# Optimization experiments

Measured on AMD Instinct MI355X. Metric: run time of the kernel, lower is better.

The kernel has to match this reference:

```python
import jax, jax.numpy as jnp
import numpy as np

# dims
B, L, H, NH, D = 512, 200, 128, 4, 32      # batch, seq_len, hidden, heads (gnn & fcb), head dim H/NH
FT, TP, IP = 32, 64, 200                    # first_taxonomy_num, taxonomy/item nodes per graph
NHOP, NB = 2, 2                             # n_hop gnn layers, gip_block_nums
SH, FH = 512, 256                           # scb_hidden_units, fcb_hidden_units
ITEMS, TAX = 100001, 2000                   # item vocab (+pad row 0), taxonomy vocab
NT, NI = B * TP, B * IP                     # total taxonomy / item nodes in batched forest
DEG_I, DEG_T = 4, 2                         # in-degree per taxonomy node for i2t / t2t edges


def _ln(x, g, b, eps=1e-8):
    m = jnp.mean(x, -1, keepdims=True)
    v = jnp.mean((x - m) ** 2, -1, keepdims=True)
    return (x - m) / jnp.sqrt(v + eps) * g + b


def _gat(src_h, dst_h, es, ed, W, al, ar, bias):
    """DGL GATConv (eval mode): shared fc, leaky_relu(0.2) scores, segment softmax,
    identity residual (in == heads*out), bias, ReLU activation."""
    fs = (src_h @ W).reshape(-1, NH, D)                 # [Ns,NH,D]
    fd = (dst_h @ W).reshape(-1, NH, D)                 # [Nd,NH,D]
    el = jnp.sum(fs * al, -1)                           # [Ns,NH]
    er = jnp.sum(fd * ar, -1)                           # [Nd,NH]
    e = jax.nn.leaky_relu(el[es] + er[ed], 0.2)         # [E,NH]
    emax = jax.ops.segment_max(e, ed, num_segments=NT)
    a = jnp.exp(e - emax[ed])
    s = jax.ops.segment_sum(a, ed, num_segments=NT)
    alpha = a / s[ed]                                   # [E,NH]
    rst = jax.ops.segment_sum(alpha[..., None] * fs[es], ed, num_segments=NT)
    rst = rst + dst_h.reshape(-1, NH, D) + bias.reshape(NH, D)
    return jax.nn.relu(rst).reshape(-1, NH * D)


def _forward(item_embed, tax_embed, scb_ln_g, scb_ln_b, scb_w1, scb_w2, fcb_ln_g, fcb_ln_b,
             fcb_w1, fcb_w2, fcb_w3, wv, gi_w, gi_al, gi_ar, gi_b, gt_w, gt_al, gt_ar, gt_b,
             liw_g, liw_b, int_g, int_b, uni_w,
             seq, root, i2t_src, i2t_dst, t2t_src, t2t_dst, item_ids, tax_ids):
    # --- global intention: mixer-style blocks over the item sequence ---
    V = item_embed[seq]                                           # [B,L,H]
    for i in range(NB):
        nv = _ln(V, scb_ln_g[i], scb_ln_b[i])
        t = jax.nn.gelu(jnp.einsum('blh,ls->bhs', nv, scb_w1[i]), approximate=False)
        vs = nv + jnp.einsum('bhs,sl->blh', t, scb_w2[i])         # seq-mixing block
        nvs = _ln(vs, fcb_ln_g[i], fcb_ln_b[i])
        xh = nvs.reshape(B, L, NH, D)                             # fcb heads share w1/w2
        y = jax.nn.gelu(jnp.einsum('blkc,cf->blkf', xh, fcb_w1[i]), approximate=False)
        y = jnp.einsum('blkf,fc->blkc', y, fcb_w2[i]).reshape(B, L, H)
        V = nvs + y @ fcb_w3[i]
    alpha = jax.nn.softmax(V @ wv, axis=1)                        # [B,L]
    g = jnp.sum(alpha[..., None] * V, axis=1)                     # [B,H]
    # --- local intention: multi-hop hetero GAT on batched item-taxonomy forest ---
    item_h = item_embed[item_ids]                                 # [NI,H]
    tax_h = tax_embed[tax_ids]                                    # [NT,H]
    acc = jnp.zeros_like(tax_h)
    for hop in range(NHOP):
        t_i = _gat(item_h, tax_h, i2t_src, i2t_dst, gi_w[hop], gi_al[hop], gi_ar[hop], gi_b[hop])
        t_t = _gat(tax_h, tax_h, t2t_src, t2t_dst, gt_w[hop], gt_al[hop], gt_ar[hop], gt_b[hop])
        tax_h = t_i + t_t                                         # HeteroGraphConv 'sum'
        acc = acc + tax_h                                         # k_list accumulation
    total = acc / NHOP                                            # average over hops
    offs = jnp.arange(B) * TP                                     # batched-graph offsets (graph_taxonomy)
    valid = root != -1
    local = jnp.where(valid[..., None], total[jnp.clip(root, 0) + offs[:, None]], 0.0)  # [B,FT,H]
    # --- fuse global + local ---
    mul = jnp.einsum('bfh,bh->bf', local, g)                      # [B,FT]
    w = jax.nn.softmax(jnp.where(mul != 0, _ln(mul, liw_g, liw_b), -jnp.inf), axis=-1)
    intention = _ln(g + jnp.sum(w[..., None] * local, axis=1), int_g, int_b)
    return (intention @ uni_w) @ item_embed.T                     # [B, ITEMS]


def setup_inputs():
    key = jax.random.key(0)
    ks = jax.random.split(key, 32)
    nrm = lambda i, sh: jax.random.normal(ks[i], sh, jnp.float32) * 0.05
    inp = {}
    inp['seq'] = jax.random.randint(ks[0], (B, L), 0, ITEMS)
    inp['root'] = jax.random.randint(ks[1], (B, FT), 0, TP)       # all valid roots
    i2t_dst = jnp.repeat(jnp.arange(NT), DEG_I)
    inp['i2t_dst'] = i2t_dst
    inp['i2t_src'] = (i2t_dst // TP) * IP + jax.random.randint(ks[2], (NT * DEG_I,), 0, IP)
    t2t_dst = jnp.repeat(jnp.arange(NT), DEG_T)
    inp['t2t_dst'] = t2t_dst
    inp['t2t_src'] = (t2t_dst // TP) * TP + jax.random.randint(ks[3], (NT * DEG_T,), 0, TP)
    inp['item_ids'] = jax.random.randint(ks[4], (NI,), 1, ITEMS)
    inp['tax_ids'] = jax.random.randint(ks[5], (NT,), 1, TAX)
    inp['item_embed'] = nrm(6, (ITEMS, H)).at[0].set(0.0)         # padding_idx=0
    inp['tax_embed'] = nrm(7, (TAX, H)).at[0].set(0.0)
    inp['scb_ln_g'] = jnp.ones((NB, H)); inp['scb_ln_b'] = jnp.zeros((NB, H))
    inp['scb_w1'] = nrm(8, (NB, L, SH)); inp['scb_w2'] = nrm(9, (NB, SH, L))
    inp['fcb_ln_g'] = jnp.ones((NB, H)); inp['fcb_ln_b'] = jnp.zeros((NB, H))
    inp['fcb_w1'] = nrm(10, (NB, D, FH)); inp['fcb_w2'] = nrm(11, (NB, FH, D))
    inp['fcb_w3'] = nrm(12, (NB, H, H))
    inp['wv'] = nrm(13, (H,))
    inp['gi_w'] = nrm(14, (NHOP, H, H)); inp['gi_al'] = nrm(15, (NHOP, NH, D))
    inp['gi_ar'] = nrm(16, (NHOP, NH, D)); inp['gi_b'] = nrm(17, (NHOP, H))
    inp['gt_w'] = nrm(18, (NHOP, H, H)); inp['gt_al'] = nrm(19, (NHOP, NH, D))
    inp['gt_ar'] = nrm(20, (NHOP, NH, D)); inp['gt_b'] = nrm(21, (NHOP, H))
    inp['liw_g'] = jnp.ones((FT,)); inp['liw_b'] = jnp.zeros((FT,))
    inp['int_g'] = jnp.ones((H,)); inp['int_b'] = jnp.zeros((H,))
    inp['uni_w'] = nrm(22, (H, H))
    return inp


def reference(item_embed, tax_embed, scb_ln_g, scb_ln_b, scb_w1, scb_w2, fcb_ln_g, fcb_ln_b,
              fcb_w1, fcb_w2, fcb_w3, wv, gi_w, gi_al, gi_ar, gi_b, gt_w, gt_al, gt_ar, gt_b,
              liw_g, liw_b, int_g, int_b, uni_w,
              seq, root, i2t_src, i2t_dst, t2t_src, t2t_dst, item_ids, tax_ids):
    return _forward(item_embed, tax_embed, scb_ln_g, scb_ln_b, scb_w1, scb_w2, fcb_ln_g, fcb_ln_b,
                    fcb_w1, fcb_w2, fcb_w3, wv, gi_w, gi_al, gi_ar, gi_b, gt_w, gt_al, gt_ar, gt_b,
                    liw_g, liw_b, int_g, int_b, uni_w,
                    seq, root, i2t_src, i2t_dst, t2t_src, t2t_dst, item_ids, tax_ids)
```

## Files before the change

kernel.cpp:

```cpp
#include <hip/hip_runtime.h>
#include <hip/hip_bf16.h>

constexpr int TB = 512, TL = 200, TH = 128, TNH = 4, TD = 32;
constexpr int TFT = 32, TTP = 64, TIP = 200;
constexpr int TSH = 512, TFH = 256;
constexpr int TITEMS = 100001;
constexpr int TNT = TB * TTP;
constexpr int TNI = TB * TIP;
constexpr int TLP = 224;
constexpr int TIPAD = 100096;

typedef __attribute__((ext_vector_type(8))) short short8v;
typedef __attribute__((ext_vector_type(4))) float f32x4;

__device__ inline float gelu_fast(float x) {
    float u = x + 0.044715f * x * x * x;
    float e = exp2f(-2.302208f * u);
    return x / (1.0f + e);
}
__device__ inline unsigned short to_bf16u(float x) {
    __hip_bfloat16 h = __float2bfloat16(x);
    return *reinterpret_cast<unsigned short*>(&h);
}
__device__ inline float bfu_to_f(unsigned short u) {
    unsigned int x = ((unsigned int)u) << 16;
    return __uint_as_float(x);
}

__device__ inline float block_reduce_sum(float v, float* red) {
    for (int o = 32; o > 0; o >>= 1) v += __shfl_down(v, o, 64);
    int nw = blockDim.x >> 6;
    if ((threadIdx.x & 63) == 0) red[threadIdx.x >> 6] = v;
    __syncthreads();
    float r = 0.f;
    for (int w = 0; w < nw; ++w) r += red[w];
    __syncthreads();
    return r;
}

__global__ __launch_bounds__(256) void k_gather(const float* __restrict__ tab,
                                                const int* __restrict__ idx,
                                                float* __restrict__ out, int nrows) {
    int e = blockIdx.x * blockDim.x + threadIdx.x;
    if (e >= nrows * 32) return;
    int r = e >> 5, c = e & 31;
    ((float4*)out)[e] = ((const float4*)tab)[(size_t)idx[r] * 32 + c];
}

__global__ __launch_bounds__(256) void k_gather_bf(const float* __restrict__ tab,
                                                   const int* __restrict__ idx,
                                                   unsigned short* __restrict__ out, int nrows) {
    int e = blockIdx.x * blockDim.x + threadIdx.x;
    if (e >= nrows * 16) return;
    int r = e >> 4, c = e & 15;
    const float4 a = ((const float4*)tab)[(size_t)idx[r] * 32 + c * 2];
    const float4 b = ((const float4*)tab)[(size_t)idx[r] * 32 + c * 2 + 1];
    uint4 u;
    u.x = (unsigned int)to_bf16u(a.x) | ((unsigned int)to_bf16u(a.y) << 16);
    u.y = (unsigned int)to_bf16u(a.z) | ((unsigned int)to_bf16u(a.w) << 16);
    u.z = (unsigned int)to_bf16u(b.x) | ((unsigned int)to_bf16u(b.y) << 16);
    u.w = (unsigned int)to_bf16u(b.z) | ((unsigned int)to_bf16u(b.w) << 16);
    *(uint4*)(out + (size_t)e * 8) = u;
}

__global__ __launch_bounds__(256) void k_wcvt(const float* __restrict__ fw1, const float* __restrict__ fw2,
                                              const float* __restrict__ fw3, const float* __restrict__ giw,
                                              const float* __restrict__ gtw, unsigned short* __restrict__ WB) {
    int idx = blockIdx.x * 256 + threadIdx.x;
    float v;
    if (idx < 16384) {
        int nb = idx >> 13, r = idx & 8191, n = r >> 5, k = r & 31;
        v = fw1[(size_t)nb * 8192 + k * 256 + n];
    } else if (idx < 32768) {
        int t = idx - 16384;
        int nb = t >> 13, r = t & 8191, n = r >> 8, k = r & 255;
        v = fw2[(size_t)nb * 8192 + k * 32 + n];
    } else if (idx < 65536) {
        int t = idx - 32768;
        int nb = t >> 14, r = t & 16383, n = r >> 7, k = r & 127;
        v = fw3[(size_t)nb * 16384 + k * 128 + n];
    } else if (idx < 98304) {
        int t = idx - 65536;
        int hop = t >> 14, r = t & 16383, n = r >> 7, k = r & 127;
        v = giw[(size_t)hop * 16384 + k * 128 + n];
    } else {
        int t = idx - 98304;
        int hop = t >> 14, r = t & 16383, n = r >> 7, k = r & 127;
        v = gtw[(size_t)hop * 16384 + k * 128 + n];
    }
    WB[idx] = to_bf16u(v);
}

__global__ __launch_bounds__(128) void k_lnt(const float* __restrict__ V,
                                             const float* __restrict__ g, const float* __restrict__ b,
                                             float* __restrict__ NV, unsigned short* __restrict__ NVT) {
    __shared__ float tl[64][129];
    __shared__ float mrow[64], irow[64];
    int bb = blockIdx.y, l0 = blockIdx.x * 64, tid = threadIdx.x;
    for (int i = tid; i < 2048; i += 128) {
        int r = i >> 5, c = i & 31;
        int l = l0 + r;
        float4 v = {0.f, 0.f, 0.f, 0.f};
        if (l < TL) v = *(const float4*)(V + ((size_t)bb * TL + l) * TH + c * 4);
        tl[r][c * 4 + 0] = v.x; tl[r][c * 4 + 1] = v.y;
        tl[r][c * 4 + 2] = v.z; tl[r][c * 4 + 3] = v.w;
    }
    __syncthreads();
    {
        int row = tid >> 1, half = tid & 1;
        float s = 0.f, sq = 0.f;
        for (int k = 0; k < 64; ++k) {
            float v = tl[row][half * 64 + k];
            s += v; sq += v * v;
        }
        s += __shfl_xor(s, 1);
        sq += __shfl_xor(sq, 1);
        if (half == 0) {
            float mean = s * (1.f / 128.f);
            mrow[row] = mean;
            irow[row] = rsqrtf(sq * (1.f / 128.f) - mean * mean + 1e-8f);
        }
    }
    __syncthreads();
    for (int i = tid; i < 2048; i += 128) {
        int r = i >> 5, c = i & 31;
        int l = l0 + r;
        float4 o = {0.f, 0.f, 0.f, 0.f};
        if (l < TL) {
            float4 v = *(float4*)&tl[r][c * 4];
            float m = mrow[r], inv = irow[r];
            const float4 gg = ((const float4*)g)[c];
            const float4 bv = ((const float4*)b)[c];
            o.x = (v.x - m) * inv * gg.x + bv.x;
            o.y = (v.y - m) * inv * gg.y + bv.y;
            o.z = (v.z - m) * inv * gg.z + bv.z;
            o.w = (v.w - m) * inv * gg.w + bv.w;
            *(float4*)(NV + ((size_t)bb * TL + l) * TH + c * 4) = o;
        }
        *(float4*)&tl[r][c * 4] = o;
    }
    __syncthreads();
    int h = tid;
    int ng = (l0 + 64 > TLP) ? (TLP - l0) / 8 : 8;
    for (int lg = 0; lg < ng; ++lg) {
        uint4 u;
        unsigned int p[4];
#pragma unroll
        for (int q = 0; q < 4; ++q) {
            unsigned short ua = to_bf16u(tl[lg * 8 + q * 2 + 0][h]);
            unsigned short ub = to_bf16u(tl[lg * 8 + q * 2 + 1][h]);
            p[q] = (unsigned int)ua | ((unsigned int)ub << 16);
        }
        u.x = p[0]; u.y = p[1]; u.z = p[2]; u.w = p[3];
        *(uint4*)(NVT + ((size_t)bb * TH + h) * TLP + l0 + lg * 8) = u;
    }
}

__global__ __launch_bounds__(256) void k_wscb(const float* __restrict__ w1, const float* __restrict__ w2,
                                              unsigned short* __restrict__ W1T,
                                              unsigned short* __restrict__ W2T) {
    int bx = blockIdx.x;
    if (bx < TSH) {
        int s = bx, l = threadIdx.x;
        if (l < TLP) W1T[(size_t)s * TLP + l] = to_bf16u(l < TL ? w1[(size_t)l * TSH + s] : 0.f);
    } else {
        int l = bx - TSH;
        for (int it = 0; it < 2; ++it) {
            int s = it * 256 + threadIdx.x;
            W2T[(size_t)l * TSH + s] = to_bf16u(l < TL ? w2[(size_t)s * TL + l] : 0.f);
        }
    }
}

__global__ __launch_bounds__(256) void k_mm1(const unsigned short* __restrict__ NVT,
                                             const unsigned short* __restrict__ W1T,
                                             unsigned short* __restrict__ T, int bh) {
    __shared__ unsigned short As[128][40];
    __shared__ unsigned short Bs[128][40];
    int tid = threadIdx.x;
    int b_local = blockIdx.y, b = bh * 256 + b_local;
    int s0 = blockIdx.x * 128;
    int lane = tid & 63, wid = tid >> 6;
    int mw = wid >> 1, nw = wid & 1;
    f32x4 acc[4][4];
#pragma unroll
    for (int i = 0; i < 4; ++i)
#pragma unroll
        for (int j = 0; j < 4; ++j) acc[i][j] = (f32x4){0.f, 0.f, 0.f, 0.f};
    const unsigned short* Abase = NVT + (size_t)b * TH * TLP;
    const unsigned short* Bbase = W1T + (size_t)s0 * TLP;
    for (int kc = 0; kc < 7; ++kc) {
        __syncthreads();
        for (int i = tid; i < 512; i += 256) {
            int r = i >> 2, q = i & 3;
            *(uint4*)&As[r][q * 8] = *(const uint4*)(Abase + (size_t)r * TLP + kc * 32 + q * 8);
            *(uint4*)&Bs[r][q * 8] = *(const uint4*)(Bbase + (size_t)r * TLP + kc * 32 + q * 8);
        }
        __syncthreads();
        int ko = (lane >> 4) * 8;
        short8v af[4], bfr[4];
#pragma unroll
        for (int t = 0; t < 4; ++t) {
            af[t] = *(const short8v*)&As[mw * 64 + t * 16 + (lane & 15)][ko];
            bfr[t] = *(const short8v*)&Bs[nw * 64 + t * 16 + (lane & 15)][ko];
        }
#pragma unroll
        for (int i = 0; i < 4; ++i)
#pragma unroll
            for (int j = 0; j < 4; ++j)
                acc[i][j] = __builtin_amdgcn_mfma_f32_16x16x32_bf16(af[i], bfr[j], acc[i][j], 0, 0, 0);
    }
    int rbase = (lane >> 4) * 4, col = lane & 15;
#pragma unroll
    for (int i = 0; i < 4; ++i)
#pragma unroll
        for (int j = 0; j < 4; ++j) {
            int h0 = mw * 64 + i * 16 + rbase;
            int s = s0 + nw * 64 + j * 16 + col;
#pragma unroll
            for (int r = 0; r < 4; ++r)
                T[((size_t)b_local * TH + h0 + r) * TSH + s] = to_bf16u(gelu_fast(acc[i][j][r]));
        }
}

__global__ __launch_bounds__(256) void k_mm2l(const unsigned short* __restrict__ T,
                                              const unsigned short* __restrict__ W2T,
                                              float* __restrict__ NV,
                                              const float* __restrict__ lg, const float* __restrict__ lb,
                                              int bh) {
    __shared__ unsigned short As[128][40];
    __shared__ unsigned short Bs[64][40];
    __shared__ float vsl[64][132];
    __shared__ float mrow[64], irow[64];
    int tid = threadIdx.x;
    int b_local = blockIdx.y, b = bh * 256 + b_local;
    int l0 = blockIdx.x * 64;
    int lane = tid & 63, wid = tid >> 6;
    f32x4 acc[2][4];
#pragma unroll
    for (int i = 0; i < 2; ++i)
#pragma unroll
        for (int j = 0; j < 4; ++j) acc[i][j] = (f32x4){0.f, 0.f, 0.f, 0.f};
    const unsigned short* Abase = T + (size_t)b_local * TH * TSH;
    for (int kc = 0; kc < 16; ++kc) {
        __syncthreads();
        for (int i = tid; i < 512; i += 256) {
            int r = i >> 2, q = i & 3;
            *(uint4*)&As[r][q * 8] = *(const uint4*)(Abase + (size_t)r * TSH + kc * 32 + q * 8);
        }
        {
            int r = tid >> 2, q = tid & 3;
            int l = l0 + r;
            uint4 v = {0u, 0u, 0u, 0u};
            if (l < 208) v = *(const uint4*)(W2T + (size_t)l * TSH + kc * 32 + q * 8);
            *(uint4*)&Bs[r][q * 8] = v;
        }
        __syncthreads();
        int ko = (lane >> 4) * 8;
        short8v af[2], bfr[4];
#pragma unroll
        for (int t = 0; t < 2; ++t)
            af[t] = *(const short8v*)&As[wid * 32 + t * 16 + (lane & 15)][ko];
#pragma unroll
        for (int j = 0; j < 4; ++j)
            bfr[j] = *(const short8v*)&Bs[j * 16 + (lane & 15)][ko];
#pragma unroll
        for (int i = 0; i < 2; ++i)
#pragma unroll
            for (int j = 0; j < 4; ++j)
                acc[i][j] = __builtin_amdgcn_mfma_f32_16x16x32_bf16(af[i], bfr[j], acc[i][j], 0, 0, 0);
    }
    int rbase = (lane >> 4) * 4, col = lane & 15;
#pragma unroll
    for (int i = 0; i < 2; ++i)
#pragma unroll
        for (int j = 0; j < 4; ++j) {
            int l = l0 + j * 16 + col;
            int h0 = wid * 32 + i * 16 + rbase;
            float4 res = {0.f, 0.f, 0.f, 0.f};
            if (l < TL) res = *(const float4*)(NV + ((size_t)b * TL + l) * TH + h0);
            vsl[j * 16 + col][h0 + 0] = acc[i][j][0] + res.x;
            vsl[j * 16 + col][h0 + 1] = acc[i][j][1] + res.y;
            vsl[j * 16 + col][h0 + 2] = acc[i][j][2] + res.z;
            vsl[j * 16 + col][h0 + 3] = acc[i][j][3] + res.w;
        }
    __syncthreads();
    int row = tid >> 2, q = tid & 3;
    {
        float s = 0.f, sq = 0.f;
        for (int k = 0; k < 32; ++k) {
            float v = vsl[row][q * 32 + k];
            s += v; sq += v * v;
        }
        s += __shfl_xor(s, 1); s += __shfl_xor(s, 2);
        sq += __shfl_xor(sq, 1); sq += __shfl_xor(sq, 2);
        if (q == 0) {
            float mean = s * (1.f / 128.f);
            mrow[row] = mean;
            irow[row] = rsqrtf(sq * (1.f / 128.f) - mean * mean + 1e-8f);
        }
    }
    __syncthreads();
    {
        int l = l0 + row;
        if (l < TL) {
            float mean = mrow[row], inv = irow[row];
            float* dst = NV + ((size_t)b * TL + l) * TH + q * 32;
#pragma unroll
            for (int k4 = 0; k4 < 8; ++k4) {
                float4 v = *(float4*)&vsl[row][q * 32 + k4 * 4];
                const float4 gg = ((const float4*)lg)[q * 8 + k4];
                const float4 bv = ((const float4*)lb)[q * 8 + k4];
                float4 o;
                o.x = (v.x - mean) * inv * gg.x + bv.x;
                o.y = (v.y - mean) * inv * gg.y + bv.y;
                o.z = (v.z - mean) * inv * gg.z + bv.z;
                o.w = (v.w - mean) * inv * gg.w + bv.w;
                *(float4*)(dst + k4 * 4) = o;
            }
        }
    }
}

__global__ __launch_bounds__(256) void k_ffuse(const float* __restrict__ NV,
                                               const unsigned short* __restrict__ FW1B,
                                               const unsigned short* __restrict__ FW2B,
                                               unsigned short* __restrict__ Z) {
    __shared__ unsigned short As[64][40];
    __shared__ unsigned short BsBuf[256 * 40];
    __shared__ unsigned short Yl[64 * 264];
    int tid = threadIdx.x;
    int m0 = blockIdx.x * 64;
    int lane = tid & 63, wid = tid >> 6;
    for (int i = tid; i < 512; i += 256) {
        int r = i >> 3, q = i & 7;
        const float4 v = *(const float4*)(NV + (size_t)(m0 + r) * 32 + q * 4);
        ushort4 u;
        u.x = to_bf16u(v.x); u.y = to_bf16u(v.y); u.z = to_bf16u(v.z); u.w = to_bf16u(v.w);
        *(ushort4*)&As[r][q * 4] = u;
    }
    for (int i = tid; i < 1024; i += 256) {
        int r = i >> 2, q = i & 3;
        *(uint4*)&BsBuf[r * 40 + q * 8] = *(const uint4*)(FW1B + r * 32 + q * 8);
    }
    __syncthreads();
    int ko = (lane >> 4) * 8;
    short8v af[4], bfr[4];
#pragma unroll
    for (int t = 0; t < 4; ++t) {
        af[t] = *(const short8v*)&As[t * 16 + (lane & 15)][ko];
        bfr[t] = *(const short8v*)&BsBuf[(wid * 64 + t * 16 + (lane & 15)) * 40 + ko];
    }
    __syncthreads();
    {
        f32x4 acc[4][4];
#pragma unroll
        for (int i = 0; i < 4; ++i)
#pragma unroll
            for (int j = 0; j < 4; ++j) acc[i][j] = (f32x4){0.f, 0.f, 0.f, 0.f};
#pragma unroll
        for (int i = 0; i < 4; ++i)
#pragma unroll
            for (int j = 0; j < 4; ++j)
                acc[i][j] = __builtin_amdgcn_mfma_f32_16x16x32_bf16(af[i], bfr[j], acc[i][j], 0, 0, 0);
        int rbase = (lane >> 4) * 4, col = lane & 15;
#pragma unroll
        for (int i = 0; i < 4; ++i)
#pragma unroll
            for (int j = 0; j < 4; ++j)
#pragma unroll
                for (int r = 0; r < 4; ++r) {
                    int m = i * 16 + rbase + r;
                    int n = wid * 64 + j * 16 + col;
                    int idx = (m * 264 + n) ^ (((m >> 2) & 7) << 3);
                    Yl[idx] = to_bf16u(gelu_fast(acc[i][j][r]));
                }
    }
    for (int i = tid; i < 1024; i += 256) {
        int r = i >> 5, q = i & 31;
        *(uint4*)&BsBuf[r * 264 + q * 8] = *(const uint4*)(FW2B + r * 256 + q * 8);
    }
    __syncthreads();
    {
        f32x4 acc2[2];
        acc2[0] = (f32x4){0.f, 0.f, 0.f, 0.f};
        acc2[1] = (f32x4){0.f, 0.f, 0.f, 0.f};
        int mrow = wid * 16 + (lane & 15);
        int sw = ((mrow >> 2) & 7) << 3;
        for (int kc = 0; kc < 8; ++kc) {
            int ko2 = kc * 32 + (lane >> 4) * 8;
            short8v a2 = *(const short8v*)&Yl[(mrow * 264 + ko2) ^ sw];
            short8v b0 = *(const short8v*)&BsBuf[(lane & 15) * 264 + ko2];
            short8v b1 = *(const short8v*)&BsBuf[(16 + (lane & 15)) * 264 + ko2];
            acc2[0] = __builtin_amdgcn_mfma_f32_16x16x32_bf16(a2, b0, acc2[0], 0, 0, 0);
            acc2[1] = __builtin_amdgcn_mfma_f32_16x16x32_bf16(a2, b1, acc2[1], 0, 0, 0);
        }
        int rbase = (lane >> 4) * 4, col = lane & 15;
#pragma unroll
        for (int j = 0; j < 2; ++j)
#pragma unroll
            for (int r = 0; r < 4; ++r)
                Z[(size_t)(m0 + wid * 16 + rbase + r) * 32 + j * 16 + col] =
                    to_bf16u(acc2[j][r]);
    }
}

__global__ __launch_bounds__(256) void k_gmm_b(const unsigned short* __restrict__ A,
                                               const unsigned short* __restrict__ WB,
                                               const float* __restrict__ R,
                                               float* __restrict__ C) {
    __shared__ unsigned short As[128][40];
    __shared__ unsigned short Bs[128][40];
    int tid = threadIdx.x;
    int m0 = blockIdx.x * 128;
    int lane = tid & 63, wid = tid >> 6;
    int mw = wid >> 1, nw = wid & 1;
    f32x4 acc[4][4];
#pragma unroll
    for (int i = 0; i < 4; ++i)
#pragma unroll
        for (int j = 0; j < 4; ++j) acc[i][j] = (f32x4){0.f, 0.f, 0.f, 0.f};
    for (int kc = 0; kc < 4; ++kc) {
        __syncthreads();
        for (int i = tid; i < 512; i += 256) {
            int r = i >> 2, q = i & 3;
            *(uint4*)&As[r][q * 8] = *(const uint4*)(A + (size_t)(m0 + r) * TH + kc * 32 + q * 8);
            *(uint4*)&Bs[r][q * 8] = *(const uint4*)(WB + (size_t)r * TH + kc * 32 + q * 8);
        }
        __syncthreads();
        int ko = (lane >> 4) * 8;
        short8v af[4], bfr[4];
#pragma unroll
        for (int t = 0; t < 4; ++t) {
            af[t] = *(const short8v*)&As[mw * 64 + t * 16 + (lane & 15)][ko];
            bfr[t] = *(const short8v*)&Bs[nw * 64 + t * 16 + (lane & 15)][ko];
        }
#pragma unroll
        for (int i = 0; i < 4; ++i)
#pragma unroll
            for (int j = 0; j < 4; ++j)
                acc[i][j] = __builtin_amdgcn_mfma_f32_16x16x32_bf16(af[i], bfr[j], acc[i][j], 0, 0, 0);
    }
    int rbase = (lane >> 4) * 4, col = lane & 15;
#pragma unroll
    for (int i = 0; i < 4; ++i)
#pragma unroll
        for (int j = 0; j < 4; ++j) {
            int n = nw * 64 + j * 16 + col;
#pragma unroll
            for (int r = 0; r < 4; ++r) {
                size_t off = (size_t)(m0 + mw * 64 + i * 16 + rbase + r) * TH + n;
                float v = acc[i][j][r];
                if (R) v += R[off];
                C[off] = v;
            }
        }
}

__global__ __launch_bounds__(256) void k_gmm_bb(const unsigned short* __restrict__ A,
                                                const unsigned short* __restrict__ WB,
                                                unsigned short* __restrict__ C) {
    __shared__ unsigned short As[128][40];
    __shared__ unsigned short Bs[128][40];
    int tid = threadIdx.x;
    int m0 = blockIdx.x * 128;
    int lane = tid & 63, wid = tid >> 6;
    int mw = wid >> 1, nw = wid & 1;
    f32x4 acc[4][4];
#pragma unroll
    for (int i = 0; i < 4; ++i)
#pragma unroll
        for (int j = 0; j < 4; ++j) acc[i][j] = (f32x4){0.f, 0.f, 0.f, 0.f};
    for (int kc = 0; kc < 4; ++kc) {
        __syncthreads();
        for (int i = tid; i < 512; i += 256) {
            int r = i >> 2, q = i & 3;
            *(uint4*)&As[r][q * 8] = *(const uint4*)(A + (size_t)(m0 + r) * TH + kc * 32 + q * 8);
            *(uint4*)&Bs[r][q * 8] = *(const uint4*)(WB + (size_t)r * TH + kc * 32 + q * 8);
        }
        __syncthreads();
        int ko = (lane >> 4) * 8;
        short8v af[4], bfr[4];
#pragma unroll
        for (int t = 0; t < 4; ++t) {
            af[t] = *(const short8v*)&As[mw * 64 + t * 16 + (lane & 15)][ko];
            bfr[t] = *(const short8v*)&Bs[nw * 64 + t * 16 + (lane & 15)][ko];
        }
#pragma unroll
        for (int i = 0; i < 4; ++i)
#pragma unroll
            for (int j = 0; j < 4; ++j)
                acc[i][j] = __builtin_amdgcn_mfma_f32_16x16x32_bf16(af[i], bfr[j], acc[i][j], 0, 0, 0);
    }
    int rbase = (lane >> 4) * 4, col = lane & 15;
#pragma unroll
    for (int i = 0; i < 4; ++i)
#pragma unroll
        for (int j = 0; j < 4; ++j) {
            int n = nw * 64 + j * 16 + col;
#pragma unroll
            for (int r = 0; r < 4; ++r) {
                size_t off = (size_t)(m0 + mw * 64 + i * 16 + rbase + r) * TH + n;
                C[off] = to_bf16u(acc[i][j][r]);
            }
        }
}

__global__ __launch_bounds__(256) void k_pool(const float* __restrict__ V, const float* __restrict__ wv,
                                              float* __restrict__ g) {
    __shared__ float sc[TL];
    __shared__ float red[4];
    int b = blockIdx.x, tid = threadIdx.x;
    if (tid < TL) {
        float a = 0.f;
        const float* vp = V + (size_t)(b * TL + tid) * TH;
        for (int h = 0; h < TH; ++h) a += vp[h] * wv[h];
        sc[tid] = a;
    }
    __syncthreads();
    float m = (tid < TL) ? sc[tid] : -INFINITY;
    for (int o = 32; o > 0; o >>= 1) m = fmaxf(m, __shfl_down(m, o, 64));
    if ((tid & 63) == 0) red[tid >> 6] = m;
    __syncthreads();
    m = fmaxf(fmaxf(red[0], red[1]), fmaxf(red[2], red[3]));
    __syncthreads();
    float e = (tid < TL) ? expf(sc[tid] - m) : 0.f;
    float s = block_reduce_sum(e, red);
    if (tid < TL) sc[tid] = e / s;
    __syncthreads();
    if (tid < TH) {
        float a = 0.f;
        for (int l = 0; l < TL; ++l) a += sc[l] * V[(size_t)(b * TL + l) * TH + tid];
        g[b * TH + tid] = a;
    }
}

__global__ __launch_bounds__(256) void k_scores4(
        const unsigned short* __restrict__ f0, const float* __restrict__ v0, float* __restrict__ o0, int n0,
        const unsigned short* __restrict__ f1, const float* __restrict__ v1, float* __restrict__ o1, int n1,
        const unsigned short* __restrict__ f2, const float* __restrict__ v2, float* __restrict__ o2, int n2,
        const unsigned short* __restrict__ f3, const float* __restrict__ v3, float* __restrict__ o3, int n3) {
    int t = blockIdx.x * 256 + threadIdx.x;
    const unsigned short* f; const float* vec; float* o;
    if (t < n0 * 4) { f = f0; vec = v0; o = o0; }
    else {
        t -= n0 * 4;
        if (t < n1 * 4) { f = f1; vec = v1; o = o1; }
        else {
            t -= n1 * 4;
            if (t < n2 * 4) { f = f2; vec = v2; o = o2; }
            else {
                t -= n2 * 4;
                if (t >= n3 * 4) return;
                f = f3; vec = v3; o = o3;
            }
        }
    }
    int node = t >> 2, k = t & 3;
    const unsigned short* fp = f + (size_t)node * TH + k * TD;
    const float* vp = vec + k * TD;
    float a = 0.f;
#pragma unroll
    for (int q = 0; q < 4; ++q) {
        uint4 u = *(const uint4*)(fp + q * 8);
        unsigned int ws[4] = {u.x, u.y, u.z, u.w};
#pragma unroll
        for (int p = 0; p < 4; ++p) {
            a += __uint_as_float(ws[p] << 16) * vp[q * 8 + p * 2];
            a += __uint_as_float(ws[p] & 0xffff0000u) * vp[q * 8 + p * 2 + 1];
        }
    }
    o[t] = a;
}

__global__ __launch_bounds__(128) void k_gat(const unsigned short* __restrict__ tax_cur,
                                             const unsigned short* __restrict__ fs_i, const float* __restrict__ el_i,
                                             const float* __restrict__ er_i, const int* __restrict__ src_i,
                                             const float* __restrict__ bi,
                                             const unsigned short* __restrict__ fs_t, const float* __restrict__ el_t,
                                             const float* __restrict__ er_t, const int* __restrict__ src_t,
                                             const float* __restrict__ bt,
                                             unsigned short* __restrict__ tax_nxt,
                                             float* __restrict__ acc, int hop) {
    int n = blockIdx.x, h = threadIdx.x, k = h >> 5;
    float cur = bfu_to_f(tax_cur[(size_t)n * TH + h]);
    float ti, tt2;
    {
        float er = er_i[n * 4 + k];
        int s[4]; float e[4]; float m = -INFINITY;
#pragma unroll
        for (int j = 0; j < 4; ++j) {
            s[j] = src_i[n * 4 + j];
            float xx = el_i[s[j] * 4 + k] + er;
            e[j] = xx > 0.f ? xx : 0.2f * xx;
            m = fmaxf(m, e[j]);
        }
        float ssum = 0.f, av = 0.f;
#pragma unroll
        for (int j = 0; j < 4; ++j) {
            float a = expf(e[j] - m);
            ssum += a;
            av += a * bfu_to_f(fs_i[(size_t)s[j] * TH + h]);
        }
        ti = fmaxf(av / ssum + cur + bi[h], 0.f);
    }
    {
        float er = er_t[n * 4 + k];
        int s[2]; float e[2]; float m = -INFINITY;
#pragma unroll
        for (int j = 0; j < 2; ++j) {
            s[j] = src_t[n * 2 + j];
            float xx = el_t[s[j] * 4 + k] + er;
            e[j] = xx > 0.f ? xx : 0.2f * xx;
            m = fmaxf(m, e[j]);
        }
        float ssum = 0.f, av = 0.f;
#pragma unroll
        for (int j = 0; j < 2; ++j) {
            float a = expf(e[j] - m);
            ssum += a;
            av += a * bfu_to_f(fs_t[(size_t)s[j] * TH + h]);
        }
        tt2 = fmaxf(av / ssum + cur + bt[h], 0.f);
    }
    float nx = ti + tt2;
    size_t ai = (size_t)n * TH + h;
    tax_nxt[ai] = to_bf16u(nx);
    acc[ai] = (hop == 0) ? nx : acc[ai] + nx;
}

__global__ __launch_bounds__(128) void k_locfuse(const int* __restrict__ root, const float* __restrict__ acc,
                                                 const float* __restrict__ g,
                                                 const float* __restrict__ liw_g, const float* __restrict__ liw_b,
                                                 const float* __restrict__ int_g, const float* __restrict__ int_b,
                                                 const float* __restrict__ uni_w,
                                                 unsigned short* __restrict__ PB) {
    __shared__ float loc[TFT][TH];
    __shared__ float lm[TFT], wv_[TFT], inten[TH];
    __shared__ float red[2];
    int b = blockIdx.x, tid = threadIdx.x;
    float gv = g[b * TH + tid];
    for (int f = 0; f < TFT; ++f) {
        int r = root[b * TFT + f];
        float v = 0.f;
        if (r != -1) v = acc[(size_t)(b * TTP + (r < 0 ? 0 : r)) * TH + tid] * 0.5f;
        loc[f][tid] = v;
        float s = block_reduce_sum(v * gv, red);
        if (tid == 0) lm[f] = s;
    }
    __syncthreads();
    if (tid < TFT) {
        float mean = 0.f;
        for (int f = 0; f < TFT; ++f) mean += lm[f];
        mean *= (1.f / TFT);
        float var = 0.f;
        for (int f = 0; f < TFT; ++f) { float d = lm[f] - mean; var += d * d; }
        var *= (1.f / TFT);
        float ln = (lm[tid] - mean) * rsqrtf(var + 1e-8f) * liw_g[tid] + liw_b[tid];
        wv_[tid] = (lm[tid] != 0.f) ? ln : -INFINITY;
    }
    __syncthreads();
    if (tid < TFT) {
        float mx = -INFINITY;
        for (int f = 0; f < TFT; ++f) mx = fmaxf(mx, wv_[f]);
        float s = 0.f;
        for (int f = 0; f < TFT; ++f) s += expf(wv_[f] - mx);
        lm[tid] = expf(wv_[tid] - mx) / s;
    }
    __syncthreads();
    float ip = gv;
    for (int f = 0; f < TFT; ++f) ip += lm[f] * loc[f][tid];
    float mean = block_reduce_sum(ip, red) * (1.f / TH);
    float d = ip - mean;
    float var = block_reduce_sum(d * d, red) * (1.f / TH);
    inten[tid] = d * rsqrtf(var + 1e-8f) * int_g[tid] + int_b[tid];
    __syncthreads();
    float a = 0.f;
    for (int hp = 0; hp < TH; ++hp) a += inten[hp] * uni_w[hp * TH + tid];
    PB[(size_t)b * TH + tid] = to_bf16u(a);
}

__global__ __launch_bounds__(256) void k_ebc(const float* __restrict__ E,
                                             unsigned short* __restrict__ EB) {
    int t = blockIdx.x * 256 + threadIdx.x;
    if (t >= TIPAD * TH / 8) return;
    size_t base = (size_t)t * 8;
    int row = (int)(base >> 7);
    float4 a = {0.f, 0.f, 0.f, 0.f}, b = {0.f, 0.f, 0.f, 0.f};
    if (row < TITEMS) {
        a = *(const float4*)(E + base);
        b = *(const float4*)(E + base + 4);
    }
    ushort4 u0, u1;
    u0.x = to_bf16u(a.x); u0.y = to_bf16u(a.y); u0.z = to_bf16u(a.z); u0.w = to_bf16u(a.w);
    u1.x = to_bf16u(b.x); u1.y = to_bf16u(b.y); u1.z = to_bf16u(b.z); u1.w = to_bf16u(b.w);
    *(ushort4*)(EB + base) = u0;
    *(ushort4*)(EB + base + 4) = u1;
}

__global__ __launch_bounds__(256) void k_final_m(const unsigned short* __restrict__ PB,
                                                 const unsigned short* __restrict__ EB,
                                                 float* __restrict__ out) {
    __shared__ unsigned short Bs[128][136];
    int tid = threadIdx.x;
    int i0 = blockIdx.x * 128, b0 = blockIdx.y * 128;
    for (int i = tid; i < 2048; i += 256) {
        int r = i >> 4, q = i & 15;
        *(uint4*)&Bs[r][q * 8] = *(const uint4*)(EB + (size_t)(i0 + r) * TH + q * 8);
    }
    __syncthreads();
    int lane = tid & 63, wid = tid >> 6;
    int mw = wid >> 1, nw = wid & 1;
    f32x4 acc[4][4];
#pragma unroll
    for (int i = 0; i < 4; ++i)
#pragma unroll
        for (int j = 0; j < 4; ++j) acc[i][j] = (f32x4){0.f, 0.f, 0.f, 0.f};
#pragma unroll
    for (int kc = 0; kc < 4; ++kc) {
        int ko = kc * 32 + (lane >> 4) * 8;
        short8v af[4], bfr[4];
#pragma unroll
        for (int t = 0; t < 4; ++t) {
            af[t] = *(const short8v*)(PB + (size_t)(b0 + mw * 64 + t * 16 + (lane & 15)) * TH + ko);
            bfr[t] = *(const short8v*)&Bs[nw * 64 + t * 16 + (lane & 15)][ko];
        }
#pragma unroll
        for (int i = 0; i < 4; ++i)
#pragma unroll
            for (int j = 0; j < 4; ++j)
                acc[i][j] = __builtin_amdgcn_mfma_f32_16x16x32_bf16(af[i], bfr[j], acc[i][j], 0, 0, 0);
    }
    int rbase = (lane >> 4) * 4, col = lane & 15;
#pragma unroll
    for (int i = 0; i < 4; ++i)
#pragma unroll
        for (int j = 0; j < 4; ++j) {
            int ii = i0 + nw * 64 + j * 16 + col;
            if (ii < TITEMS) {
#pragma unroll
                for (int r = 0; r < 4; ++r)
                    out[(size_t)(b0 + mw * 64 + i * 16 + rbase + r) * TITEMS + ii] = acc[i][j][r];
            }
        }
}

extern "C" void kernel_launch(void* const* d_in, const int* in_sizes, int n_in,
                              void* d_out, int out_size, void* d_ws, size_t ws_size,
                              hipStream_t stream) {
    const int*   seq        = (const int*)d_in[0];
    const int*   root       = (const int*)d_in[1];
    const int*   i2t_src    = (const int*)d_in[3];
    const int*   t2t_src    = (const int*)d_in[5];
    const int*   item_ids   = (const int*)d_in[6];
    const int*   tax_ids    = (const int*)d_in[7];
    const float* item_embed = (const float*)d_in[8];
    const float* tax_embed  = (const float*)d_in[9];
    const float* scb_ln_g   = (const float*)d_in[10];
    const float* scb_ln_b   = (const float*)d_in[11];
    const float* scb_w1     = (const float*)d_in[12];
    const float* scb_w2     = (const float*)d_in[13];
    const float* fcb_ln_g   = (const float*)d_in[14];
    const float* fcb_ln_b   = (const float*)d_in[15];
    const float* fcb_w1     = (const float*)d_in[16];
    const float* fcb_w2     = (const float*)d_in[17];
    const float* fcb_w3     = (const float*)d_in[18];
    const float* wv         = (const float*)d_in[19];
    const float* gi_w       = (const float*)d_in[20];
    const float* gi_al      = (const float*)d_in[21];
    const float* gi_ar      = (const float*)d_in[22];
    const float* gi_b       = (const float*)d_in[23];
    const float* gt_w       = (const float*)d_in[24];
    const float* gt_al      = (const float*)d_in[25];
    const float* gt_ar      = (const float*)d_in[26];
    const float* gt_b       = (const float*)d_in[27];
    const float* liw_g      = (const float*)d_in[28];
    const float* liw_b      = (const float*)d_in[29];
    const float* int_g      = (const float*)d_in[30];
    const float* int_b      = (const float*)d_in[31];
    const float* uni_w      = (const float*)d_in[32];

    char* w = (char*)d_ws;
    float* V     = (float*)(w + 0);
    float* NV    = (float*)(w + 52428800);
    unsigned short* FSIB   = (unsigned short*)(w + 0);
    unsigned short* ITEMHB = (unsigned short*)(w + 52428800);
    unsigned short* NVT = (unsigned short*)(w + 104857600);
    unsigned short* T   = (unsigned short*)(w + 134217728);
    unsigned short* W1T = (unsigned short*)(w + 167772160);
    unsigned short* W2T = (unsigned short*)(w + 168001536);
    unsigned short* ZB  = (unsigned short*)(w + 104857600);
    unsigned short* TAXB0 = (unsigned short*)(w + 104857600);
    unsigned short* TAXB1 = (unsigned short*)(w + 113246208);
    float* ACC   = (float*)(w + 138412032);
    unsigned short* FDIB = (unsigned short*)(w + 155189248);
    unsigned short* FSTB = (unsigned short*)(w + 171966464);
    float* ELI   = (float*)(w + 188743680);
    float* ERI   = (float*)(w + 190382080);
    float* ELT   = (float*)(w + 190906368);
    float* ERT   = (float*)(w + 191430656);
    float* G     = (float*)(w + 200343552);
    unsigned short* WB = (unsigned short*)(w + 191954944);
    unsigned short* EB = (unsigned short*)(w + 155189248);
    unsigned short* PB = (unsigned short*)(w + 200671232);
    if (ws_size < 200933376ull) return;

    k_wcvt<<<512, 256, 0, stream>>>(fcb_w1, fcb_w2, fcb_w3, gi_w, gt_w, WB);

    k_gather<<<(TB * TL * 32 + 255) / 256, 256, 0, stream>>>(item_embed, seq, V, TB * TL);
    for (int nb = 0; nb < 2; ++nb) {
        k_lnt<<<dim3(4, TB), 128, 0, stream>>>(V, scb_ln_g + nb * TH, scb_ln_b + nb * TH, NV, NVT);
        k_wscb<<<720, 256, 0, stream>>>(scb_w1 + nb * TL * TSH, scb_w2 + nb * TSH * TL, W1T, W2T);
        for (int bh = 0; bh < 2; ++bh) {
            k_mm1<<<dim3(4, 256), 256, 0, stream>>>(NVT, W1T, T, bh);
            k_mm2l<<<dim3(4, 256), 256, 0, stream>>>(T, W2T, NV,
                                                     fcb_ln_g + nb * TH, fcb_ln_b + nb * TH, bh);
        }
        k_ffuse<<<TB * TL * 4 / 64, 256, 0, stream>>>(NV, WB + nb * 8192, WB + 16384 + nb * 8192, ZB);
        k_gmm_b<<<TB * TL / 128, 256, 0, stream>>>(ZB, WB + 32768 + nb * 16384, NV, V);
    }
    k_pool<<<TB, 256, 0, stream>>>(V, wv, G);

    k_gather_bf<<<(TNI * 16 + 255) / 256, 256, 0, stream>>>(item_embed, item_ids, ITEMHB, TNI);
    k_gather_bf<<<(TNT * 16 + 255) / 256, 256, 0, stream>>>(tax_embed, tax_ids, TAXB0, TNT);

    unsigned short* curb = TAXB0;
    unsigned short* nxtb = TAXB1;
    for (int hop = 0; hop < 2; ++hop) {
        const unsigned short* WiB = WB + 65536 + hop * 16384;
        const unsigned short* WtB = WB + 98304 + hop * 16384;
        k_gmm_bb<<<TNI / 128, 256, 0, stream>>>(ITEMHB, WiB, FSIB);
        k_gmm_bb<<<TNT / 128, 256, 0, stream>>>(curb, WiB, FDIB);
        k_gmm_bb<<<TNT / 128, 256, 0, stream>>>(curb, WtB, FSTB);
        int total = (TNI + 3 * TNT) * TNH;
        k_scores4<<<(total + 255) / 256, 256, 0, stream>>>(
            FSIB, gi_al + hop * TH, ELI, TNI,
            FDIB, gi_ar + hop * TH, ERI, TNT,
            FSTB, gt_al + hop * TH, ELT, TNT,
            FSTB, gt_ar + hop * TH, ERT, TNT);
        k_gat<<<TNT, 128, 0, stream>>>(curb, FSIB, ELI, ERI, i2t_src, gi_b + hop * TH,
                                       FSTB, ELT, ERT, t2t_src, gt_b + hop * TH, nxtb, ACC, hop);
        unsigned short* tmp = curb; curb = nxtb; nxtb = tmp;
    }

    k_locfuse<<<TB, 128, 0, stream>>>(root, ACC, G, liw_g, liw_b, int_g, int_b, uni_w, PB);
    k_ebc<<<(TIPAD * TH / 8 + 255) / 256, 256, 0, stream>>>(item_embed, EB);
    k_final_m<<<dim3(TIPAD / 128, TB / 128), 256, 0, stream>>>(PB, EB, (float*)d_out);
}
```

Measured before the change: 1.033 ms.

## Fold fcb w2·w3 into one matrix and fuse the FCB block into one kernel

Precomputes the product of fcb_w2 and the per-head slice of fcb_w3 into a bf16 matrix, so the FCB block becomes gelu(X·W1) times that merged matrix plus the residual, all in one kernel. This removes the intermediate Z buffer and the separate k_gmm_b launch, trading them for a larger K=256 second GEMM per head. GEMM epilogues are also transposed (operands swapped in the MFMA) so each lane writes packed 4-element vectors instead of scalar stores. Folding the weights changes the bf16 rounding points, so numerics may drift slightly.

```diff
diff --git a/kernel.cpp b/kernel.cpp
--- a/kernel.cpp
+++ b/kernel.cpp
@@ -91,6 +91,20 @@
     WB[idx] = to_bf16u(v);
 }
 
+__global__ __launch_bounds__(128) void k_mprep(const float* __restrict__ fw2,
+                                               const float* __restrict__ fw3,
+                                               unsigned short* __restrict__ MfT) {
+    int bx = blockIdx.x;
+    int nb = bx >> 10, kk = (bx >> 8) & 3, f = bx & 255;
+    int h = threadIdx.x;
+    const float* w2p = fw2 + (size_t)nb * 8192 + f * 32;
+    const float* w3p = fw3 + (size_t)nb * 16384 + kk * 32 * 128 + h;
+    float a = 0.f;
+#pragma unroll
+    for (int c = 0; c < 32; ++c) a += w2p[c] * w3p[c * 128];
+    MfT[(((size_t)nb * 4 + kk) * 128 + h) * 256 + f] = to_bf16u(a);
+}
+
 __global__ __launch_bounds__(128) void k_lnt(const float* __restrict__ V,
                                              const float* __restrict__ g, const float* __restrict__ b,
                                              float* __restrict__ NV, unsigned short* __restrict__ NVT) {
@@ -182,11 +196,11 @@
     int s0 = blockIdx.x * 128;
     int lane = tid & 63, wid = tid >> 6;
     int mw = wid >> 1, nw = wid & 1;
-    f32x4 acc[4][4];
-#pragma unroll
-    for (int i = 0; i < 4; ++i)
-#pragma unroll
-        for (int j = 0; j < 4; ++j) acc[i][j] = (f32x4){0.f, 0.f, 0.f, 0.f};
+    f32x4 accT[4][4];
+#pragma unroll
+    for (int j = 0; j < 4; ++j)
+#pragma unroll
+        for (int i = 0; i < 4; ++i) accT[j][i] = (f32x4){0.f, 0.f, 0.f, 0.f};
     const unsigned short* Abase = NVT + (size_t)b * TH * TLP;
     const unsigned short* Bbase = W1T + (size_t)s0 * TLP;
     for (int kc = 0; kc < 7; ++kc) {
@@ -205,21 +219,24 @@
             bfr[t] = *(const short8v*)&Bs[nw * 64 + t * 16 + (lane & 15)][ko];
         }
 #pragma unroll
-        for (int i = 0; i < 4; ++i)
-#pragma unroll
-            for (int j = 0; j < 4; ++j)
-                acc[i][j] = __builtin_amdgcn_mfma_f32_16x16x32_bf16(af[i], bfr[j], acc[i][j], 0, 0, 0);
+        for (int j = 0; j < 4; ++j)
+#pragma unroll
+            for (int i = 0; i < 4; ++i)
+                accT[j][i] = __builtin_amdgcn_mfma_f32_16x16x32_bf16(bfr[j], af[i], accT[j][i], 0, 0, 0);
     }
     int rbase = (lane >> 4) * 4, col = lane & 15;
 #pragma unroll
     for (int i = 0; i < 4; ++i)
 #pragma unroll
         for (int j = 0; j < 4; ++j) {
-            int h0 = mw * 64 + i * 16 + rbase;
-            int s = s0 + nw * 64 + j * 16 + col;
-#pragma unroll
-            for (int r = 0; r < 4; ++r)
-                T[((size_t)b_local * TH + h0 + r) * TSH + s] = to_bf16u(gelu_fast(acc[i][j][r]));
+            int h = mw * 64 + i * 16 + col;
+            int sb = s0 + nw * 64 + j * 16 + rbase;
+            ushort4 pk;
+            pk.x = to_bf16u(gelu_fast(accT[j][i][0]));
+            pk.y = to_bf16u(gelu_fast(accT[j][i][1]));
+            pk.z = to_bf16u(gelu_fast(accT[j][i][2]));
+            pk.w = to_bf16u(gelu_fast(accT[j][i][3]));
+            *(ushort4*)(T + ((size_t)b_local * TH + h) * TSH + sb) = pk;
         }
 }
 
@@ -279,10 +296,12 @@
             int h0 = wid * 32 + i * 16 + rbase;
             float4 res = {0.f, 0.f, 0.f, 0.f};
             if (l < TL) res = *(const float4*)(NV + ((size_t)b * TL + l) * TH + h0);
-            vsl[j * 16 + col][h0 + 0] = acc[i][j][0] + res.x;
-            vsl[j * 16 + col][h0 + 1] = acc[i][j][1] + res.y;
-            vsl[j * 16 + col][h0 + 2] = acc[i][j][2] + res.z;
-            vsl[j * 16 + col][h0 + 3] = acc[i][j][3] + res.w;
+            float4 o;
+            o.x = acc[i][j][0] + res.x;
+            o.y = acc[i][j][1] + res.y;
+            o.z = acc[i][j][2] + res.z;
+            o.w = acc[i][j][3] + res.w;
+            *(float4*)&vsl[j * 16 + col][h0] = o;
         }
     __syncthreads();
     int row = tid >> 2, q = tid & 3;
@@ -322,139 +341,92 @@
     }
 }
 
-__global__ __launch_bounds__(256) void k_ffuse(const float* __restrict__ NV,
-                                               const unsigned short* __restrict__ FW1B,
-                                               const unsigned short* __restrict__ FW2B,
-                                               unsigned short* __restrict__ Z) {
-    __shared__ unsigned short As[64][40];
-    __shared__ unsigned short BsBuf[256 * 40];
+__global__ __launch_bounds__(256) void k_ffuse2(const float* __restrict__ NV,
+                                                const unsigned short* __restrict__ FW1B,
+                                                const unsigned short* __restrict__ MfT,
+                                                float* __restrict__ V) {
+    __shared__ unsigned short Xb[64 * 136];
     __shared__ unsigned short Yl[64 * 264];
+    __shared__ unsigned short Bs2[128 * 40];
     int tid = threadIdx.x;
     int m0 = blockIdx.x * 64;
     int lane = tid & 63, wid = tid >> 6;
-    for (int i = tid; i < 512; i += 256) {
-        int r = i >> 3, q = i & 7;
-        const float4 v = *(const float4*)(NV + (size_t)(m0 + r) * 32 + q * 4);
+    int col = lane & 15, rbase = (lane >> 4) * 4, ko = (lane >> 4) * 8;
+    for (int i = tid; i < 2048; i += 256) {
+        int r = i >> 5, c = i & 31;
+        const float4 v = *(const float4*)(NV + (size_t)(m0 + r) * TH + c * 4);
         ushort4 u;
         u.x = to_bf16u(v.x); u.y = to_bf16u(v.y); u.z = to_bf16u(v.z); u.w = to_bf16u(v.w);
-        *(ushort4*)&As[r][q * 4] = u;
-    }
-    for (int i = tid; i < 1024; i += 256) {
-        int r = i >> 2, q = i & 3;
-        *(uint4*)&BsBuf[r * 40 + q * 8] = *(const uint4*)(FW1B + r * 32 + q * 8);
-    }
-    __syncthreads();
-    int ko = (lane >> 4) * 8;
-    short8v af[4], bfr[4];
-#pragma unroll
-    for (int t = 0; t < 4; ++t) {
-        af[t] = *(const short8v*)&As[t * 16 + (lane & 15)][ko];
-        bfr[t] = *(const short8v*)&BsBuf[(wid * 64 + t * 16 + (lane & 15)) * 40 + ko];
-    }
-    __syncthreads();
-    {
-        f32x4 acc[4][4];
-#pragma unroll
-        for (int i = 0; i < 4; ++i)
-#pragma unroll
-            for (int j = 0; j < 4; ++j) acc[i][j] = (f32x4){0.f, 0.f, 0.f, 0.f};
-#pragma unroll
-        for (int i = 0; i < 4; ++i)
+        *(ushort4*)&Xb[r * 136 + c * 4] = u;
+    }
+    __syncthreads();
+    f32x4 acc[8];
+#pragma unroll
+    for (int t = 0; t < 8; ++t) acc[t] = (f32x4){0.f, 0.f, 0.f, 0.f};
+    int mrow = wid * 16 + col;
+    int sw = ((mrow >> 2) & 7) << 3;
+    for (int head = 0; head < 4; ++head) {
+        {
+            short8v af[4], bfr[4];
+#pragma unroll
+            for (int i = 0; i < 4; ++i)
+                af[i] = *(const short8v*)&Xb[(i * 16 + col) * 136 + head * 32 + ko];
 #pragma unroll
             for (int j = 0; j < 4; ++j)
-                acc[i][j] = __builtin_amdgcn_mfma_f32_16x16x32_bf16(af[i], bfr[j], acc[i][j], 0, 0, 0);
-        int rbase = (lane >> 4) * 4, col = lane & 15;
-#pragma unroll
-        for (int i = 0; i < 4; ++i)
+                bfr[j] = *(const short8v*)(FW1B + (size_t)(wid * 64 + j * 16 + col) * 32 + ko);
+            f32x4 yt[4][4];
 #pragma unroll
             for (int j = 0; j < 4; ++j)
 #pragma unroll
-                for (int r = 0; r < 4; ++r) {
-                    int m = i * 16 + rbase + r;
-                    int n = wid * 64 + j * 16 + col;
-                    int idx = (m * 264 + n) ^ (((m >> 2) & 7) << 3);
-                    Yl[idx] = to_bf16u(gelu_fast(acc[i][j][r]));
+                for (int i = 0; i < 4; ++i) yt[j][i] = (f32x4){0.f, 0.f, 0.f, 0.f};
+#pragma unroll
+            for (int j = 0; j < 4; ++j)
+#pragma unroll
+                for (int i = 0; i < 4; ++i)
+                    yt[j][i] = __builtin_amdgcn_mfma_f32_16x16x32_bf16(bfr[j], af[i], yt[j][i], 0, 0, 0);
+#pragma unroll
+            for (int i = 0; i < 4; ++i)
+#pragma unroll
+                for (int j = 0; j < 4; ++j) {
+                    int m = i * 16 + col;
+                    int n0 = wid * 64 + j * 16 + rbase;
+                    ushort4 pk;
+                    pk.x = to_bf16u(gelu_fast(yt[j][i][0]));
+                    pk.y = to_bf16u(gelu_fast(yt[j][i][1]));
+                    pk.z = to_bf16u(gelu_fast(yt[j][i][2]));
+                    pk.w = to_bf16u(gelu_fast(yt[j][i][3]));
+                    int idx = (m * 264 + n0) ^ (((m >> 2) & 7) << 3);
+                    *(ushort4*)&Yl[idx] = pk;
                 }
-    }
-    for (int i = tid; i < 1024; i += 256) {
-        int r = i >> 5, q = i & 31;
-        *(uint4*)&BsBuf[r * 264 + q * 8] = *(const uint4*)(FW2B + r * 256 + q * 8);
-    }
-    __syncthreads();
-    {
-        f32x4 acc2[2];
-        acc2[0] = (f32x4){0.f, 0.f, 0.f, 0.f};
-        acc2[1] = (f32x4){0.f, 0.f, 0.f, 0.f};
-        int mrow = wid * 16 + (lane & 15);
-        int sw = ((mrow >> 2) & 7) << 3;
+        }
         for (int kc = 0; kc < 8; ++kc) {
-            int ko2 = kc * 32 + (lane >> 4) * 8;
-            short8v a2 = *(const short8v*)&Yl[(mrow * 264 + ko2) ^ sw];
-            short8v b0 = *(const short8v*)&BsBuf[(lane & 15) * 264 + ko2];
-            short8v b1 = *(const short8v*)&BsBuf[(16 + (lane & 15)) * 264 + ko2];
-            acc2[0] = __builtin_amdgcn_mfma_f32_16x16x32_bf16(a2, b0, acc2[0], 0, 0, 0);
-            acc2[1] = __builtin_amdgcn_mfma_f32_16x16x32_bf16(a2, b1, acc2[1], 0, 0, 0);
-        }
-        int rbase = (lane >> 4) * 4, col = lane & 15;
-#pragma unroll
-        for (int j = 0; j < 2; ++j)
-#pragma unroll
-            for (int r = 0; r < 4; ++r)
-                Z[(size_t)(m0 + wid * 16 + rbase + r) * 32 + j * 16 + col] =
-                    to_bf16u(acc2[j][r]);
-    }
-}
-
-__global__ __launch_bounds__(256) void k_gmm_b(const unsigned short* __restrict__ A,
-                                               const unsigned short* __restrict__ WB,
-                                               const float* __restrict__ R,
-                                               float* __restrict__ C) {
-    __shared__ unsigned short As[128][40];
-    __shared__ unsigned short Bs[128][40];
-    int tid = threadIdx.x;
-    int m0 = blockIdx.x * 128;
-    int lane = tid & 63, wid = tid >> 6;
-    int mw = wid >> 1, nw = wid & 1;
-    f32x4 acc[4][4];
-#pragma unroll
-    for (int i = 0; i < 4; ++i)
-#pragma unroll
-        for (int j = 0; j < 4; ++j) acc[i][j] = (f32x4){0.f, 0.f, 0.f, 0.f};
-    for (int kc = 0; kc < 4; ++kc) {
-        __syncthreads();
-        for (int i = tid; i < 512; i += 256) {
-            int r = i >> 2, q = i & 3;
-            *(uint4*)&As[r][q * 8] = *(const uint4*)(A + (size_t)(m0 + r) * TH + kc * 32 + q * 8);
-            *(uint4*)&Bs[r][q * 8] = *(const uint4*)(WB + (size_t)r * TH + kc * 32 + q * 8);
-        }
-        __syncthreads();
-        int ko = (lane >> 4) * 8;
-        short8v af[4], bfr[4];
-#pragma unroll
-        for (int t = 0; t < 4; ++t) {
-            af[t] = *(const short8v*)&As[mw * 64 + t * 16 + (lane & 15)][ko];
-            bfr[t] = *(const short8v*)&Bs[nw * 64 + t * 16 + (lane & 15)][ko];
-        }
-#pragma unroll
-        for (int i = 0; i < 4; ++i)
-#pragma unroll
-            for (int j = 0; j < 4; ++j)
-                acc[i][j] = __builtin_amdgcn_mfma_f32_16x16x32_bf16(af[i], bfr[j], acc[i][j], 0, 0, 0);
-    }
-    int rbase = (lane >> 4) * 4, col = lane & 15;
-#pragma unroll
-    for (int i = 0; i < 4; ++i)
-#pragma unroll
-        for (int j = 0; j < 4; ++j) {
-            int n = nw * 64 + j * 16 + col;
-#pragma unroll
-            for (int r = 0; r < 4; ++r) {
-                size_t off = (size_t)(m0 + mw * 64 + i * 16 + rbase + r) * TH + n;
-                float v = acc[i][j][r];
-                if (R) v += R[off];
-                C[off] = v;
+            for (int i = tid; i < 512; i += 256) {
+                int r = i >> 2, q = i & 3;
+                *(uint4*)&Bs2[r * 40 + q * 8] =
+                    *(const uint4*)(MfT + ((size_t)head * 128 + r) * 256 + kc * 32 + q * 8);
             }
-        }
+            __syncthreads();
+            short8v a2 = *(const short8v*)&Yl[(mrow * 264 + kc * 32 + ko) ^ sw];
+#pragma unroll
+            for (int t = 0; t < 8; ++t) {
+                short8v b2 = *(const short8v*)&Bs2[(t * 16 + col) * 40 + ko];
+                acc[t] = __builtin_amdgcn_mfma_f32_16x16x32_bf16(b2, a2, acc[t], 0, 0, 0);
+            }
+            __syncthreads();
+        }
+    }
+    int m = m0 + wid * 16 + col;
+#pragma unroll
+    for (int t = 0; t < 8; ++t) {
+        int h0 = t * 16 + rbase;
+        const float4 res = *(const float4*)(NV + (size_t)m * TH + h0);
+        float4 o;
+        o.x = acc[t][0] + res.x;
+        o.y = acc[t][1] + res.y;
+        o.z = acc[t][2] + res.z;
+        o.w = acc[t][3] + res.w;
+        *(float4*)(V + (size_t)m * TH + h0) = o;
+    }
 }
 
 __global__ __launch_bounds__(256) void k_gmm_bb(const unsigned short* __restrict__ A,
@@ -466,11 +438,11 @@
     int m0 = blockIdx.x * 128;
     int lane = tid & 63, wid = tid >> 6;
     int mw = wid >> 1, nw = wid & 1;
-    f32x4 acc[4][4];
-#pragma unroll
-    for (int i = 0; i < 4; ++i)
-#pragma unroll
-        for (int j = 0; j < 4; ++j) acc[i][j] = (f32x4){0.f, 0.f, 0.f, 0.f};
+    f32x4 accT[4][4];
+#pragma unroll
+    for (int j = 0; j < 4; ++j)
+#pragma unroll
+        for (int i = 0; i < 4; ++i) accT[j][i] = (f32x4){0.f, 0.f, 0.f, 0.f};
     for (int kc = 0; kc < 4; ++kc) {
         __syncthreads();
         for (int i = tid; i < 512; i += 256) {
@@ -487,22 +459,24 @@
             bfr[t] = *(const short8v*)&Bs[nw * 64 + t * 16 + (lane & 15)][ko];
         }
 #pragma unroll
-        for (int i = 0; i < 4; ++i)
-#pragma unroll
-            for (int j = 0; j < 4; ++j)
-                acc[i][j] = __builtin_amdgcn_mfma_f32_16x16x32_bf16(af[i], bfr[j], acc[i][j], 0, 0, 0);
+        for (int j = 0; j < 4; ++j)
+#pragma unroll
+            for (int i = 0; i < 4; ++i)
+                accT[j][i] = __builtin_amdgcn_mfma_f32_16x16x32_bf16(bfr[j], af[i], accT[j][i], 0, 0, 0);
     }
     int rbase = (lane >> 4) * 4, col = lane & 15;
 #pragma unroll
     for (int i = 0; i < 4; ++i)
 #pragma unroll
         for (int j = 0; j < 4; ++j) {
-            int n = nw * 64 + j * 16 + col;
-#pragma unroll
-            for (int r = 0; r < 4; ++r) {
-                size_t off = (size_t)(m0 + mw * 64 + i * 16 + rbase + r) * TH + n;
-                C[off] = to_bf16u(acc[i][j][r]);
-            }
+            int m = m0 + mw * 64 + i * 16 + col;
+            int n0 = nw * 64 + j * 16 + rbase;
+            ushort4 pk;
+            pk.x = to_bf16u(accT[j][i][0]);
+            pk.y = to_bf16u(accT[j][i][1]);
+            pk.z = to_bf16u(accT[j][i][2]);
+            pk.w = to_bf16u(accT[j][i][3]);
+            *(ushort4*)(C + (size_t)m * TH + n0) = pk;
         }
 }
 
@@ -789,7 +763,7 @@
     unsigned short* T   = (unsigned short*)(w + 134217728);
     unsigned short* W1T = (unsigned short*)(w + 167772160);
     unsigned short* W2T = (unsigned short*)(w + 168001536);
-    unsigned short* ZB  = (unsigned short*)(w + 104857600);
+    unsigned short* MfT = (unsigned short*)(w + 168230912);
     unsigned short* TAXB0 = (unsigned short*)(w + 104857600);
     unsigned short* TAXB1 = (unsigned short*)(w + 113246208);
     float* ACC   = (float*)(w + 138412032);
@@ -806,6 +780,7 @@
     if (ws_size < 200933376ull) return;
 
     k_wcvt<<<512, 256, 0, stream>>>(fcb_w1, fcb_w2, fcb_w3, gi_w, gt_w, WB);
+    k_mprep<<<2048, 128, 0, stream>>>(fcb_w2, fcb_w3, MfT);
 
     k_gather<<<(TB * TL * 32 + 255) / 256, 256, 0, stream>>>(item_embed, seq, V, TB * TL);
     for (int nb = 0; nb < 2; ++nb) {
@@ -816,8 +791,8 @@
             k_mm2l<<<dim3(4, 256), 256, 0, stream>>>(T, W2T, NV,
                                                      fcb_ln_g + nb * TH, fcb_ln_b + nb * TH, bh);
         }
-        k_ffuse<<<TB * TL * 4 / 64, 256, 0, stream>>>(NV, WB + nb * 8192, WB + 16384 + nb * 8192, ZB);
-        k_gmm_b<<<TB * TL / 128, 256, 0, stream>>>(ZB, WB + 32768 + nb * 16384, NV, V);
+        k_ffuse2<<<TB * TL / 64, 256, 0, stream>>>(NV, WB + nb * 8192,
+                                                   MfT + (size_t)nb * 131072, V);
     }
     k_pool<<<TB, 256, 0, stream>>>(V, wv, G);
 
```

Measured after the change: 1.082 ms. +4.8%, slower.
